# Kernel tuning notes

Measured on AMD Instinct MI355X. Metric: run time of the kernel, lower is better.

Reference implementation:

```python
import jax, jax.numpy as jnp
import numpy as np

B, S, E, A = 8, 127, 512, 256  # batch, seq (pre-sentinel), encoder dim, arc representation dim

_BRANCHES = ["sib_head", "sib_dep", "cop_head", "cop_dep", "gp_head", "gp_dep", "gp_head_dep"]


def setup_inputs() -> dict:
    key = jax.random.key(0)
    ks = jax.random.split(key, 16)
    d = {
        "x": jax.random.normal(ks[0], (B, S, E), jnp.float32),
        "pos_tags": jax.random.randint(ks[1], (B, S), 0, 48),
        "mask": jnp.ones((B, S), jnp.int32),
    }
    for i, n in enumerate(_BRANCHES):
        d[f"W_{n}"] = jax.random.normal(ks[2 + i], (E, A), jnp.float32) * (1.0 / np.sqrt(E))
        d[f"b_{n}"] = jnp.zeros((A,), jnp.float32)
    for i, n in enumerate(["sib", "cop", "gp"]):
        d[f"U_{n}"] = jax.random.normal(ks[9 + i], (A, A, A), jnp.float32) * (1.0 / A)
    d["sentinel"] = jax.random.normal(ks[12], (E,), jnp.float32)
    return d


def _tri(u, v, w, U):
    # trilinear (triaffine) score: s[b,i,j,k] = sum_{a,c,d} u[b,i,a] U[a,c,d] v[b,j,c] w[b,k,d]
    t = jnp.einsum('bia,acd->bicd', u, U)       # [B, n, A, A]
    t = jnp.einsum('bicd,bjc->bijd', t, v)      # [B, n, n, A]
    return jnp.einsum('bijd,bkd->bijk', t, w)   # [B, n, n, n]


def reference(x, pos_tags, mask,
              W_sib_head, b_sib_head, W_sib_dep, b_sib_dep,
              W_cop_head, b_cop_head, W_cop_dep, b_cop_dep,
              W_gp_head, b_gp_head, W_gp_dep, b_gp_dep,
              W_gp_head_dep, b_gp_head_dep,
              U_sib, U_cop, U_gp, sentinel):
    b, _, e = x.shape
    # prepend head sentinel token
    h = jnp.concatenate([jnp.broadcast_to(sentinel, (b, 1, e)), x], axis=1)  # [B, n, E]
    mask_full = jnp.concatenate([jnp.ones((b, 1), mask.dtype), mask], axis=1)
    elu = jax.nn.elu
    sib_head = elu(h @ W_sib_head + b_sib_head)
    sib_dep = elu(h @ W_sib_dep + b_sib_dep)
    cop_head = elu(h @ W_cop_head + b_cop_head)
    cop_dep = elu(h @ W_cop_dep + b_cop_dep)
    gp_head = elu(h @ W_gp_head + b_gp_head)
    gp_dep = elu(h @ W_gp_dep + b_gp_dep)
    gp_head_dep = elu(h @ W_gp_head_dep + b_gp_head_dep)
    sib = _tri(sib_head, sib_dep, sib_dep, U_sib)
    cop = _tri(cop_head, cop_dep, cop_head, U_cop)
    gp = _tri(gp_head, gp_head_dep, gp_dep, U_gp)
    return sib, cop, gp, mask_full
```

## Files before the change

kernel.cpp:

```cpp
#include <hip/hip_runtime.h>
#include <math.h>

#define N_TOK 128
#define ADIM  256
#define EDIM  512
#define BSZ   8
#define NSQ   65536

typedef short bf16x8 __attribute__((ext_vector_type(8)));
typedef float f32x4  __attribute__((ext_vector_type(4)));
#define MFMA_BF16(a, b, c) __builtin_amdgcn_mfma_f32_16x16x32_bf16((a), (b), (c), 0, 0, 0)

__device__ inline short f2bf(float f) {
  union { float f; unsigned u; } v; v.f = f;
  unsigned r = v.u + 0x7fff + ((v.u >> 16) & 1);
  return (short)(r >> 16);
}

typedef const __attribute__((address_space(1))) unsigned int* gas_ptr;
typedef __attribute__((address_space(3))) unsigned int* las_ptr;
__device__ __forceinline__ void gload16(const void* g, void* l) {
  __builtin_amdgcn_global_load_lds((gas_ptr)g, (las_ptr)l, 16, 0, 0);
}

struct ProjArgs {
  const float* W[7];
  const float* b[7];
};
struct UArgs {
  const float* U[3];
};

__global__ __launch_bounds__(256) void proj_kernel(
    const float* __restrict__ x, const float* __restrict__ sentinel,
    ProjArgs args, short* __restrict__ proj)
{
  const int p  = blockIdx.y;
  const int m0 = blockIdx.x * 8;
  const int tid = threadIdx.x;
  __shared__ float hs[8][EDIM];
  #pragma unroll
  for (int q = 0; q < 16; ++q) {
    int idx = tid + q * 256;
    int r = idx >> 9, c = idx & 511;
    int m = m0 + r, b = m >> 7, i = m & 127;
    hs[r][c] = (i == 0) ? sentinel[c] : x[((size_t)(b * 127) + (i - 1)) * EDIM + c];
  }
  __syncthreads();
  const float* W = args.W[p];
  float bias = args.b[p][tid];
  float acc[8];
  #pragma unroll
  for (int r = 0; r < 8; ++r) acc[r] = bias;
  #pragma unroll 4
  for (int k = 0; k < EDIM; ++k) {
    float wv = W[(size_t)k * ADIM + tid];
    #pragma unroll
    for (int r = 0; r < 8; ++r) acc[r] = fmaf(hs[r][k], wv, acc[r]);
  }
  short* outp = proj + ((size_t)p * (BSZ * N_TOK) + m0) * ADIM + tid;
  #pragma unroll
  for (int r = 0; r < 8; ++r) {
    float v = acc[r];
    v = v > 0.f ? v : expm1f(v);
    outp[(size_t)r * ADIM] = f2bf(v);
  }
}

__global__ __launch_bounds__(256) void permU_all(
    UArgs ua, short* __restrict__ UtAll)
{
  __shared__ float tile[64][69];
  const int c  = blockIdx.x;
  const int a0 = blockIdx.y * 64;
  const int z  = blockIdx.z;
  const int sc = z >> 2;
  const int d0 = (z & 3) * 64;
  const float* U = ua.U[sc];
  short* Ut = UtAll + (size_t)sc * NSQ * ADIM;
  const int t  = threadIdx.x;
  {
    int ar = t >> 4, ds4 = (t & 15) * 4;
    #pragma unroll
    for (int q = 0; q < 4; ++q) {
      int a = ar + q * 16;
      float4 v = *(const float4*)&U[(size_t)(a0 + a) * NSQ + c * 256 + d0 + ds4];
      tile[a][ds4] = v.x; tile[a][ds4 + 1] = v.y;
      tile[a][ds4 + 2] = v.z; tile[a][ds4 + 3] = v.w;
    }
  }
  __syncthreads();
  {
    int dr = t >> 4, as4 = (t & 15) * 4;
    #pragma unroll
    for (int q = 0; q < 4; ++q) {
      int d = dr + q * 16;
      ushort4 o;
      o.x = (unsigned short)f2bf(tile[as4 + 0][d]);
      o.y = (unsigned short)f2bf(tile[as4 + 1][d]);
      o.z = (unsigned short)f2bf(tile[as4 + 2][d]);
      o.w = (unsigned short)f2bf(tile[as4 + 3][d]);
      *(ushort4*)&Ut[((size_t)(d0 + d) * 256 + c) * 256 + a0 + as4] = o;
    }
  }
}

__global__ __launch_bounds__(256) void gemm_t1(
    const short* __restrict__ A,
    const short* __restrict__ Ut,
    short* __restrict__ C)
{
  __shared__ short As[128 * 32];
  __shared__ short Bs[128 * 32];
  const int tid = threadIdx.x;
  const int wave = tid >> 6, lane = tid & 63;
  const int ln15 = lane & 15, quad = lane >> 4;
  const int h = blockIdx.x;
  const int l = (h & 7) * 512 + (h >> 3);
  const int m0 = (l & 7) * 128, n0 = (l >> 3) * 128;
  const int wm = (wave & 1) * 64, wn = (wave >> 1) * 64;
  const int q0 = tid,        r0 = q0 >> 2, s0 = (q0 & 3) ^ ((r0 >> 1) & 3);
  const int q1 = tid + 256,  r1 = q1 >> 2, s1 = (q1 & 3) ^ ((r1 >> 1) & 3);
  const int rdoff = ((quad ^ ((ln15 >> 1) & 3)) << 3);
  f32x4 acc[4][4] = {};
  for (int kt = 0; kt < ADIM; kt += 32) {
    __syncthreads();
    gload16(&A [(size_t)(m0 + r0) * ADIM + kt + s0 * 8], &As[q0 * 8]);
    gload16(&A [(size_t)(m0 + r1) * ADIM + kt + s1 * 8], &As[q1 * 8]);
    gload16(&Ut[(size_t)(n0 + r0) * ADIM + kt + s0 * 8], &Bs[q0 * 8]);
    gload16(&Ut[(size_t)(n0 + r1) * ADIM + kt + s1 * 8], &Bs[q1 * 8]);
    __syncthreads();
    bf16x8 af[4], bfr[4];
    #pragma unroll
    for (int r = 0; r < 4; ++r)  af[r]  = *(bf16x8*)&As[(wm + r * 16 + ln15) * 32 + rdoff];
    #pragma unroll
    for (int c2 = 0; c2 < 4; ++c2) bfr[c2] = *(bf16x8*)&Bs[(wn + c2 * 16 + ln15) * 32 + rdoff];
    #pragma unroll
    for (int r = 0; r < 4; ++r)
      #pragma unroll
      for (int c2 = 0; c2 < 4; ++c2)
        acc[r][c2] = MFMA_BF16(bfr[c2], af[r], acc[r][c2]);
  }
  #pragma unroll
  for (int r = 0; r < 4; ++r)
    #pragma unroll
    for (int c2 = 0; c2 < 4; ++c2) {
      int m = m0 + wm + r * 16 + ln15;
      int n = n0 + wn + c2 * 16 + quad * 4;
      ushort4 o;
      o.x = (unsigned short)f2bf(acc[r][c2][0]);
      o.y = (unsigned short)f2bf(acc[r][c2][1]);
      o.z = (unsigned short)f2bf(acc[r][c2][2]);
      o.w = (unsigned short)f2bf(acc[r][c2][3]);
      *(ushort4*)&C[(size_t)m * NSQ + n] = o;
    }
}

__global__ __launch_bounds__(256) void fuse_ts(
    const short* __restrict__ t1,
    const short* __restrict__ projv,
    const short* __restrict__ projw,
    float* __restrict__ out)
{
  __shared__ short As[128 * 32];
  __shared__ short Bs[128 * 32];
  __shared__ short t2s[128 * 256];
  const int tid = threadIdx.x;
  const int wave = tid >> 6, lane = tid & 63;
  const int ln15 = lane & 15, quad = lane >> 4;
  const int i  = blockIdx.x;
  const int bl = blockIdx.y;
  const short* Bt = t1 + (size_t)(bl * N_TOK + i) * NSQ;
  const short* Av = projv + (size_t)bl * N_TOK * ADIM;
  const short* Bw = projw + (size_t)bl * N_TOK * ADIM;
  float* ob = out + (size_t)(bl * N_TOK + i) * N_TOK * N_TOK;
  const int wm = (wave & 1) * 64, wn = (wave >> 1) * 64;
  const int q0 = tid,        r0 = q0 >> 2, s0 = (q0 & 3) ^ ((r0 >> 1) & 3);
  const int q1 = tid + 256,  r1 = q1 >> 2, s1 = (q1 & 3) ^ ((r1 >> 1) & 3);
  const int rdoff = ((quad ^ ((ln15 >> 1) & 3)) << 3);

  for (int dh = 0; dh < 2; ++dh) {
    f32x4 acc[4][4] = {};
    for (int ct = 0; ct < ADIM; ct += 32) {
      __syncthreads();
      gload16(&Av[(size_t)r0 * ADIM + ct + s0 * 8],              &As[q0 * 8]);
      gload16(&Av[(size_t)r1 * ADIM + ct + s1 * 8],              &As[q1 * 8]);
      gload16(&Bt[(size_t)(dh * 128 + r0) * ADIM + ct + s0 * 8], &Bs[q0 * 8]);
      gload16(&Bt[(size_t)(dh * 128 + r1) * ADIM + ct + s1 * 8], &Bs[q1 * 8]);
      __syncthreads();
      bf16x8 af[4], bfr[4];
      #pragma unroll
      for (int r = 0; r < 4; ++r)
        af[r]  = *(bf16x8*)&As[(wm + r * 16 + ln15) * 32 + rdoff];
      #pragma unroll
      for (int c2 = 0; c2 < 4; ++c2)
        bfr[c2] = *(bf16x8*)&Bs[(wn + c2 * 16 + ln15) * 32 + rdoff];
      #pragma unroll
      for (int r = 0; r < 4; ++r)
        #pragma unroll
        for (int c2 = 0; c2 < 4; ++c2)
          acc[r][c2] = MFMA_BF16(bfr[c2], af[r], acc[r][c2]);
    }
    #pragma unroll
    for (int r = 0; r < 4; ++r)
      #pragma unroll
      for (int c2 = 0; c2 < 4; ++c2) {
        int j  = wm + r * 16 + ln15;
        int d  = dh * 128 + wn + c2 * 16 + quad * 4;
        int sp = (d >> 3) ^ (j & 7);
        ushort4 o;
        o.x = (unsigned short)f2bf(acc[r][c2][0]);
        o.y = (unsigned short)f2bf(acc[r][c2][1]);
        o.z = (unsigned short)f2bf(acc[r][c2][2]);
        o.w = (unsigned short)f2bf(acc[r][c2][3]);
        *(ushort4*)((char*)t2s + (size_t)j * 512 + sp * 16 + (quad & 1) * 8) = o;
      }
  }
  __syncthreads();

  f32x4 acc2[4][4] = {};
  for (int dt = 0; dt < ADIM; dt += 32) {
    if (dt) __syncthreads();
    gload16(&Bw[(size_t)r0 * ADIM + dt + s0 * 8], &Bs[q0 * 8]);
    gload16(&Bw[(size_t)r1 * ADIM + dt + s1 * 8], &Bs[q1 * 8]);
    __syncthreads();
    bf16x8 a2[4], b2[4];
    #pragma unroll
    for (int fr = 0; fr < 4; ++fr) {
      int j  = wm + fr * 16 + ln15;
      int sp = ((dt >> 3) + quad) ^ (j & 7);
      a2[fr] = *(bf16x8*)((char*)t2s + (size_t)j * 512 + sp * 16);
    }
    #pragma unroll
    for (int fc = 0; fc < 4; ++fc)
      b2[fc] = *(bf16x8*)&Bs[(wn + fc * 16 + ln15) * 32 + rdoff];
    #pragma unroll
    for (int fr = 0; fr < 4; ++fr)
      #pragma unroll
      for (int fc = 0; fc < 4; ++fc)
        acc2[fr][fc] = MFMA_BF16(b2[fc], a2[fr], acc2[fr][fc]);
  }
  #pragma unroll
  for (int fr = 0; fr < 4; ++fr)
    #pragma unroll
    for (int fc = 0; fc < 4; ++fc) {
      int j = wm + fr * 16 + ln15;
      int k = wn + fc * 16 + quad * 4;
      *(f32x4*)&ob[(size_t)j * N_TOK + k] = acc2[fr][fc];
    }
}

__global__ void mask_kernel(const int* __restrict__ mask, float* __restrict__ out) {
  int idx = blockIdx.x * 256 + threadIdx.x;
  if (idx < BSZ * N_TOK) {
    int b = idx >> 7, i = idx & 127;
    out[idx] = (i == 0) ? 1.0f : (float)mask[b * 127 + i - 1];
  }
}

extern "C" void kernel_launch(void* const* d_in, const int* in_sizes, int n_in,
                              void* d_out, int out_size, void* d_ws, size_t ws_size,
                              hipStream_t stream)
{
  const float* x    = (const float*)d_in[0];
  const int*   mask = (const int*)d_in[2];
  ProjArgs pa;
  for (int p = 0; p < 7; ++p) {
    pa.W[p] = (const float*)d_in[3 + 2 * p];
    pa.b[p] = (const float*)d_in[4 + 2 * p];
  }
  UArgs ua;
  ua.U[0] = (const float*)d_in[17];
  ua.U[1] = (const float*)d_in[18];
  ua.U[2] = (const float*)d_in[19];
  const float* sentinel = (const float*)d_in[20];

  short* proj = (short*)d_ws;
  const size_t ut_off = 4u << 20;
  const size_t t1_off = ut_off + 3 * ((size_t)NSQ * ADIM * 2);
  short* UtAll = (short*)((char*)d_ws + ut_off);
  short* t1    = (short*)((char*)d_ws + t1_off);

  proj_kernel<<<dim3(128, 7), 256, 0, stream>>>(x, sentinel, pa, proj);
  permU_all<<<dim3(256, 4, 12), 256, 0, stream>>>(ua, UtAll);

  const int u_idx[3] = {0, 2, 4};
  const int v_idx[3] = {1, 3, 6};
  const int w_idx[3] = {1, 2, 5};
  float* outp = (float*)d_out;

  for (int sc = 0; sc < 3; ++sc) {
    gemm_t1<<<dim3(4096), 256, 0, stream>>>(
        proj + (size_t)u_idx[sc] * 1024 * ADIM,
        UtAll + (size_t)sc * NSQ * ADIM, t1);
    fuse_ts<<<dim3(128, 8), 256, 0, stream>>>(
        t1,
        proj + (size_t)v_idx[sc] * 1024 * ADIM,
        proj + (size_t)w_idx[sc] * 1024 * ADIM,
        outp + (size_t)sc * BSZ * N_TOK * N_TOK * N_TOK);
  }
  mask_kernel<<<dim3(4), 256, 0, stream>>>(
      mask, outp + (size_t)3 * BSZ * N_TOK * N_TOK * N_TOK);
}
```

Measured before the change: 869.8 us.

## Enlarge gemm_t1 tiles to 256x256 with double-buffered LDS prefetch

```diff
diff --git a/kernel.cpp b/kernel.cpp
--- a/kernel.cpp
+++ b/kernel.cpp
@@ -105,44 +105,65 @@
   }
 }
 
-__global__ __launch_bounds__(256) void gemm_t1(
+__global__ __launch_bounds__(512) void gemm_t1(
     const short* __restrict__ A,
     const short* __restrict__ Ut,
     short* __restrict__ C)
 {
-  __shared__ short As[128 * 32];
-  __shared__ short Bs[128 * 32];
+  __shared__ short As[2][256 * 32];
+  __shared__ short Bs[2][256 * 32];
   const int tid = threadIdx.x;
   const int wave = tid >> 6, lane = tid & 63;
   const int ln15 = lane & 15, quad = lane >> 4;
   const int h = blockIdx.x;
-  const int l = (h & 7) * 512 + (h >> 3);
-  const int m0 = (l & 7) * 128, n0 = (l >> 3) * 128;
-  const int wm = (wave & 1) * 64, wn = (wave >> 1) * 64;
-  const int q0 = tid,        r0 = q0 >> 2, s0 = (q0 & 3) ^ ((r0 >> 1) & 3);
-  const int q1 = tid + 256,  r1 = q1 >> 2, s1 = (q1 & 3) ^ ((r1 >> 1) & 3);
+  const int l = (h & 7) * 128 + (h >> 3);
+  const int m0 = (l & 3) * 256, n0 = (l >> 2) * 256;
+  const int wm = (wave & 1) * 128, wn = (wave >> 1) * 64;
+  int rw[2], sw[2], qq[2];
+  #pragma unroll
+  for (int p = 0; p < 2; ++p) {
+    qq[p] = tid + p * 512;
+    rw[p] = qq[p] >> 2;
+    sw[p] = (qq[p] & 3) ^ ((rw[p] >> 1) & 3);
+  }
   const int rdoff = ((quad ^ ((ln15 >> 1) & 3)) << 3);
-  f32x4 acc[4][4] = {};
+  f32x4 acc[8][4] = {};
+  #pragma unroll
+  for (int p = 0; p < 2; ++p) {
+    gload16(&A [(size_t)(m0 + rw[p]) * ADIM + sw[p] * 8], &As[0][qq[p] * 8]);
+    gload16(&Ut[(size_t)(n0 + rw[p]) * ADIM + sw[p] * 8], &Bs[0][qq[p] * 8]);
+  }
+  __syncthreads();
+  int cur = 0;
   for (int kt = 0; kt < ADIM; kt += 32) {
+    if (kt + 32 < ADIM) {
+      #pragma unroll
+      for (int p = 0; p < 2; ++p) {
+        gload16(&A [(size_t)(m0 + rw[p]) * ADIM + kt + 32 + sw[p] * 8], &As[cur ^ 1][qq[p] * 8]);
+        gload16(&Ut[(size_t)(n0 + rw[p]) * ADIM + kt + 32 + sw[p] * 8], &Bs[cur ^ 1][qq[p] * 8]);
+      }
+    }
+    bf16x8 bfr[4];
+    #pragma unroll
+    for (int c2 = 0; c2 < 4; ++c2)
+      bfr[c2] = *(bf16x8*)&Bs[cur][(wn + c2 * 16 + ln15) * 32 + rdoff];
+    #pragma unroll
+    for (int rh = 0; rh < 2; ++rh) {
+      bf16x8 af[4];
+      #pragma unroll
+      for (int r = 0; r < 4; ++r)
+        af[r] = *(bf16x8*)&As[cur][(wm + (rh * 4 + r) * 16 + ln15) * 32 + rdoff];
+      #pragma unroll
+      for (int r = 0; r < 4; ++r)
+        #pragma unroll
+        for (int c2 = 0; c2 < 4; ++c2)
+          acc[rh * 4 + r][c2] = MFMA_BF16(bfr[c2], af[r], acc[rh * 4 + r][c2]);
+    }
     __syncthreads();
-    gload16(&A [(size_t)(m0 + r0) * ADIM + kt + s0 * 8], &As[q0 * 8]);
-    gload16(&A [(size_t)(m0 + r1) * ADIM + kt + s1 * 8], &As[q1 * 8]);
-    gload16(&Ut[(size_t)(n0 + r0) * ADIM + kt + s0 * 8], &Bs[q0 * 8]);
-    gload16(&Ut[(size_t)(n0 + r1) * ADIM + kt + s1 * 8], &Bs[q1 * 8]);
-    __syncthreads();
-    bf16x8 af[4], bfr[4];
-    #pragma unroll
-    for (int r = 0; r < 4; ++r)  af[r]  = *(bf16x8*)&As[(wm + r * 16 + ln15) * 32 + rdoff];
-    #pragma unroll
-    for (int c2 = 0; c2 < 4; ++c2) bfr[c2] = *(bf16x8*)&Bs[(wn + c2 * 16 + ln15) * 32 + rdoff];
-    #pragma unroll
-    for (int r = 0; r < 4; ++r)
-      #pragma unroll
-      for (int c2 = 0; c2 < 4; ++c2)
-        acc[r][c2] = MFMA_BF16(bfr[c2], af[r], acc[r][c2]);
-  }
-  #pragma unroll
-  for (int r = 0; r < 4; ++r)
+    cur ^= 1;
+  }
+  #pragma unroll
+  for (int r = 0; r < 8; ++r)
     #pragma unroll
     for (int c2 = 0; c2 < 4; ++c2) {
       int m = m0 + wm + r * 16 + ln15;
@@ -290,7 +311,7 @@
   float* outp = (float*)d_out;
 
   for (int sc = 0; sc < 3; ++sc) {
-    gemm_t1<<<dim3(4096), 256, 0, stream>>>(
+    gemm_t1<<<dim3(1024), 512, 0, stream>>>(
         proj + (size_t)u_idx[sc] * 1024 * ADIM,
         UtAll + (size_t)sc * NSQ * ADIM, t1);
     fuse_ts<<<dim3(128, 8), 256, 0, stream>>>(
```

Result: no change. 883.8 us (+1.6%).
